# Performance work log

Measured on AMD Instinct MI355X. Metric: run time of the kernel, lower is better.

The kernel has to match this reference:

```python
import jax, jax.numpy as jnp
import numpy as np

D_MODEL = 1024
N_HEADS = 16
D_K = D_MODEL // N_HEADS
ROPE_BASE = 10000.0


def _rope_cos_sin(seq_len, dim):
    # matches calc_rope_theta: freqs over even indices of head dim
    freqs = jnp.arange(0, dim, 2, dtype=jnp.float32) / dim
    inv_freq = 1.0 / (ROPE_BASE ** freqs)                      # [dim/2]
    pos = jnp.arange(seq_len, dtype=jnp.float32)               # [S]
    ang = pos[:, None] * inv_freq[None, :]                     # [S, dim/2]
    return jnp.cos(ang), jnp.sin(ang)


def _apply_rope(x, cos, sin):
    # x: [N, S, dk]; complex pairs are consecutive elements (view_as_complex)
    x0 = x[..., 0::2]
    x1 = x[..., 1::2]
    r = x0 * cos - x1 * sin
    i = x0 * sin + x1 * cos
    return jnp.stack([r, i], axis=-1).reshape(x.shape)


def setup_inputs() -> dict:
    key = jax.random.key(0)
    ks = jax.random.split(key, 11)
    B, S, D = 4, 1024, D_MODEL
    w = lambda k: jax.random.normal(k, (D, D), dtype=jnp.float32) * 0.02
    b = lambda k: jax.random.normal(k, (D,), dtype=jnp.float32) * 0.02
    return {
        "q": jax.random.normal(ks[0], (B, S, D), dtype=jnp.float32),
        "k": jax.random.normal(ks[1], (B, S, D), dtype=jnp.float32),
        "v": jax.random.normal(ks[2], (B, S, D), dtype=jnp.float32),
        "Wq": w(ks[3]), "bq": b(ks[4]),
        "Wk": w(ks[5]), "bk": b(ks[6]),
        "Wv": w(ks[7]), "bv": b(ks[8]),
        "Wo": w(ks[9]), "bo": b(ks[10]),
    }


def reference(q, k, v, Wq, bq, Wk, bk, Wv, bv, Wo, bo):
    B, S, D = q.shape
    H, dk = N_HEADS, D_K
    qp = (q @ Wq + bq).reshape(B, S, H, dk)
    kp = (k @ Wk + bk).reshape(B, S, H, dk)
    vp = (v @ Wv + bv).reshape(B, S, H, dk)

    cos, sin = _rope_cos_sin(S, dk)
    # Faithful to source: raw reshape (B,S,H,dk)->(-1,S,dk) before RoPE
    qp = _apply_rope(qp.reshape(-1, S, dk), cos, sin).reshape(B, S, H, dk)
    kp = _apply_rope(kp.reshape(-1, S, dk), cos, sin).reshape(B, S, H, dk)

    qh = qp.transpose(0, 2, 1, 3)  # [B,H,S,dk]
    kh = kp.transpose(0, 2, 1, 3)
    vh = vp.transpose(0, 2, 1, 3)

    scores = jnp.einsum("bhqd,bhkd->bhqk", qh, kh) / jnp.sqrt(jnp.float32(dk))
    attn = jax.nn.softmax(scores, axis=-1)
    out = jnp.einsum("bhqk,bhkd->bhqd", attn, vh)
    out = out.transpose(0, 2, 1, 3).reshape(B, S, D)
    return out @ Wo + bo
```

## Files before the change

### kernel.cpp

```cpp
#include <hip/hip_runtime.h>

typedef __attribute__((ext_vector_type(8))) short bf16x8;
typedef __attribute__((ext_vector_type(4))) short short4v;
typedef __attribute__((ext_vector_type(4))) float f32x4;
typedef __attribute__((ext_vector_type(2))) unsigned u32x2;

#define MFMA16x16x32(a, b, c) __builtin_amdgcn_mfma_f32_16x16x32_bf16((a), (b), (c), 0, 0, 0)

__device__ __forceinline__ short f2bf(float f) {
    unsigned u = __builtin_bit_cast(unsigned, f);
    u += 0x7FFFu + ((u >> 16) & 1u);
    return (short)(u >> 16);
}

__device__ __forceinline__ unsigned cvtpk(float lo, float hi) {
    unsigned r;
    asm("v_cvt_pk_bf16_f32 %0, %1, %2" : "=v"(r) : "v"(lo), "v"(hi));
    return r;
}

__device__ __forceinline__ void gl_lds16(const void* g, void* l) {
    __builtin_amdgcn_global_load_lds((__attribute__((address_space(1))) void*)g,
                                     (__attribute__((address_space(3))) void*)l,
                                     16, 0, 0);
}

__device__ __forceinline__ void cvt16(const float* __restrict__ p, bf16x8& lo, bf16x8& hi) {
    f32x4 a = *(const f32x4*)(p);
    f32x4 b = *(const f32x4*)(p + 4);
    f32x4 c = *(const f32x4*)(p + 8);
    f32x4 d = *(const f32x4*)(p + 12);
#pragma unroll
    for (int i = 0; i < 4; ++i) {
        lo[i]     = f2bf(a[i]);
        lo[i + 4] = f2bf(b[i]);
        hi[i]     = f2bf(c[i]);
        hi[i + 4] = f2bf(d[i]);
    }
}

__global__ __launch_bounds__(256) void cvt3(const float* __restrict__ x0,
                                            const float* __restrict__ x1,
                                            const float* __restrict__ x2,
                                            short* __restrict__ y) {
    int sel = blockIdx.y;
    const float* x = sel == 0 ? x0 : (sel == 1 ? x1 : x2);
    short* yy = y + (size_t)sel * (1 << 22);
    int i = (blockIdx.x * 256 + threadIdx.x) * 16;
    bf16x8 lo, hi;
    cvt16(x + i, lo, hi);
    *(bf16x8*)(yy + i)     = lo;
    *(bf16x8*)(yy + i + 8) = hi;
}

__global__ __launch_bounds__(256) void transW4(const float* __restrict__ w0,
                                               const float* __restrict__ w1,
                                               const float* __restrict__ w2,
                                               const float* __restrict__ w3,
                                               short* __restrict__ wt) {
    __shared__ short t[64][80];
    int z = blockIdx.z;
    const float* W = z == 0 ? w0 : (z == 1 ? w1 : (z == 2 ? w2 : w3));
    short* Wt = wt + (size_t)z * (1 << 20);
    int bx = blockIdx.x, by = blockIdx.y;
    int tid = threadIdx.x;
    int sr = tid >> 2, sc = (tid & 3) * 16;
    bf16x8 lo, hi;
    cvt16(W + (by * 64 + sr) * 1024 + bx * 64 + sc, lo, hi);
    *(bf16x8*)&t[sr][sc]     = lo;
    *(bf16x8*)&t[sr][sc + 8] = hi;
    __syncthreads();
    bf16x8 o0, o1;
#pragma unroll
    for (int i = 0; i < 8; ++i) {
        o0[i] = t[sc + i][sr];
        o1[i] = t[sc + 8 + i][sr];
    }
    short* dst = Wt + (bx * 64 + sr) * 1024 + by * 64 + sc;
    *(bf16x8*)(dst)     = o0;
    *(bf16x8*)(dst + 8) = o1;
}

template <int MODE, int NZ>
__global__ __launch_bounds__(512) void gemm128(const short* __restrict__ A0,
                                               const short* __restrict__ A1,
                                               const short* __restrict__ Bt0,
                                               const short* __restrict__ Bt1,
                                               const float* __restrict__ b0,
                                               const float* __restrict__ b1,
                                               void* __restrict__ d0,
                                               void* __restrict__ d1) {
    __shared__ short As[3][128 * 64];
    __shared__ short Bs[3][128 * 64];
    const int K = 1024;
    int flat = blockIdx.x;
    int xcd = flat & 7, j = flat >> 3;
    int bm = xcd * 4 + (j & 3);
    int bn = (j >> 2) & 7;
    int z  = (NZ == 2) ? (j >> 5) : 0;
    const short* A    = z ? A1 : A0;
    const short* Bt   = z ? Bt1 : Bt0;
    const float* bias = z ? b1 : b0;
    void* dstv        = z ? d1 : d0;

    int tid = threadIdx.x;
    int wave = tid >> 6, lane = tid & 63;
    int quad = lane >> 4, l16 = lane & 15;
    int wm = (wave >> 2) * 64, wn = (wave & 3) * 32;
    int swr = l16 & 7;

    f32x4 acc[4][2] = {};

    auto stage = [&](int b, int t) {
        int kb = t * 64;
#pragma unroll
        for (int jj = 0; jj < 2; ++jj) {
            int c = jj * 512 + tid;
            int row = c >> 3, sl = c & 7;
            gl_lds16(A + (bm * 128 + row) * K + kb + ((sl ^ (row & 7)) * 8),
                     &As[b][c * 8]);
        }
#pragma unroll
        for (int jj = 0; jj < 2; ++jj) {
            int c = jj * 512 + tid;
            int row = c >> 3, sl = c & 7;
            gl_lds16(Bt + (bn * 128 + row) * K + kb + ((sl ^ (row & 7)) * 8),
                     &Bs[b][c * 8]);
        }
    };

    stage(0, 0);
    stage(1, 1);

    int cur = 0;
    for (int t = 0; t < 16; ++t) {
        asm volatile("s_waitcnt vmcnt(4)" ::: "memory");
        __builtin_amdgcn_sched_barrier(0);
        __builtin_amdgcn_s_barrier();
        __builtin_amdgcn_sched_barrier(0);
        int pre = cur >= 1 ? cur - 1 : 2;
        stage(pre, (t + 2) & 15);
#pragma unroll
        for (int ks = 0; ks < 2; ++ks) {
            bf16x8 bf[2], af[4];
#pragma unroll
            for (int ni = 0; ni < 2; ++ni)
                bf[ni] = *(const bf16x8*)
                    &Bs[cur][(wn + ni * 16 + l16) * 64 + (((ks * 4 + quad) ^ swr) * 8)];
#pragma unroll
            for (int mi = 0; mi < 4; ++mi)
                af[mi] = *(const bf16x8*)
                    &As[cur][(wm + mi * 16 + l16) * 64 + (((ks * 4 + quad) ^ swr) * 8)];
            __builtin_amdgcn_s_setprio(1);
#pragma unroll
            for (int mi = 0; mi < 4; ++mi)
#pragma unroll
                for (int ni = 0; ni < 2; ++ni)
                    acc[mi][ni] = MFMA16x16x32(af[mi], bf[ni], acc[mi][ni]);
            __builtin_amdgcn_s_setprio(0);
        }
        cur = cur < 2 ? cur + 1 : 0;
    }

    int row0 = bm * 128 + wm;
    int col0 = bn * 128 + wn;
#pragma unroll
    for (int mi = 0; mi < 4; ++mi) {
#pragma unroll
        for (int ni = 0; ni < 2; ++ni) {
            int gn = col0 + ni * 16 + l16;
            float bv = bias[gn];
            f32x4 c = acc[mi][ni];
            if constexpr (MODE == 0) {
                short* dst = (short*)dstv;
                int h = gn >> 6, dd = gn & 63;
                float inv = exp2f(-(float)(dd >> 1) * 0.41524101186092029f);
#pragma unroll
                for (int r = 0; r < 4; ++r) {
                    int gm = row0 + mi * 16 + quad * 4 + r;
                    int s = gm & 1023, b = gm >> 10;
                    int p = ((s << 4) + h) & 1023;
                    float val = c[r] + bv;
                    float partner = __shfl_xor(val, 1);
                    float sn, cs;
                    __sincosf((float)p * inv, &sn, &cs);
                    float res = (dd & 1) ? fmaf(partner, sn, val * cs)
                                         : fmaf(val, cs, -(partner * sn));
                    dst[((b * 16 + h) * 1024 + s) * 64 + dd] = f2bf(res);
                }
            } else if constexpr (MODE == 2) {
                short* dst = (short*)dstv;
                int h = gn >> 6, dd = gn & 63;
                int gm0 = row0 + mi * 16 + quad * 4;
                int s0 = gm0 & 1023, b = gm0 >> 10;
                short4v pack;
#pragma unroll
                for (int r = 0; r < 4; ++r) pack[r] = f2bf(c[r] + bv);
                *(short4v*)&dst[((b * 16 + h) * 64 + dd) * 1024 + s0] = pack;
            } else {
                float* dst = (float*)dstv;
#pragma unroll
                for (int r = 0; r < 4; ++r) {
                    int gm = row0 + mi * 16 + quad * 4 + r;
                    dst[gm * 1024 + gn] = c[r] + bv;
                }
            }
        }
    }
}

__global__ __launch_bounds__(512) void attn_kernel(const short* __restrict__ Qh,
                                                   const short* __restrict__ Kh,
                                                   const short* __restrict__ Vt,
                                                   short* __restrict__ O) {
    __shared__ short Ks[2][32 * 64];
    __shared__ short Vs[2][64 * 32];
    __shared__ short Pl[8][16 * 40];
    int tid = threadIdx.x;
    int wave = tid >> 6, lane = tid & 63;
    int quad = lane >> 4, l16 = lane & 15;
    int bh = blockIdx.x & 63, qt = blockIdx.x >> 6;
    int qrow = qt * 128 + wave * 16;

    const short* Qp = Qh + (bh * 1024 + qrow) * 64;
    bf16x8 aq[2];
#pragma unroll
    for (int kh = 0; kh < 2; ++kh)
        aq[kh] = *(const bf16x8*)&Qp[l16 * 64 + kh * 32 + quad * 8];

    const short* Kp = Kh + bh * 1024 * 64;
    const short* Vp = Vt + bh * 64 * 1024;

    int ck = tid & 255;
    bool isV = tid >= 256;
    int krow = ck >> 3;
    int vrow = ck >> 2;
    int ksrc = krow * 64 + (((ck & 7) ^ (krow & 7)) * 8);
    int vsrc = vrow * 1024 + ((((ck & 3) ^ (vrow & 3) ^ ((vrow >> 2) & 3)) & 3) * 8);

    int ksw  = l16 & 7;
    int vswr = (l16 & 3) ^ ((l16 >> 2) & 3);

    float lsum = 0.f;
    f32x4 oa[4] = {};

    if (!isV) gl_lds16(Kp + ksrc, &Ks[0][ck * 8]);
    else      gl_lds16(Vp + vsrc, &Vs[0][ck * 8]);
    __syncthreads();

    short* Pw = &Pl[wave][0];

    for (int kb = 0; kb < 1024; kb += 32) {
        int cur = (kb >> 5) & 1, nxt = cur ^ 1;
        int kb2 = (kb + 32) & 1023;
        if (!isV) gl_lds16(Kp + kb2 * 64 + ksrc, &Ks[nxt][ck * 8]);
        else      gl_lds16(Vp + kb2 + vsrc,      &Vs[nxt][ck * 8]);

#pragma unroll
        for (int g = 0; g < 2; ++g) {
            f32x4 s = {};
            __builtin_amdgcn_s_setprio(1);
#pragma unroll
            for (int kh = 0; kh < 2; ++kh) {
                bf16x8 ak = *(const bf16x8*)
                    &Ks[cur][(g * 16 + l16) * 64 + (((kh * 4 + quad) ^ ksw) * 8)];
                s = MFMA16x16x32(ak, aq[kh], s);
            }
            __builtin_amdgcn_s_setprio(0);
            float p[4];
#pragma unroll
            for (int r = 0; r < 4; ++r) {
                p[r] = exp2f(s[r] * 0.18033688011112042f);
                lsum += p[r];
            }
            u32x2 w;
            w[0] = cvtpk(p[0], p[1]);
            w[1] = cvtpk(p[2], p[3]);
            *(u32x2*)&Pw[l16 * 40 + g * 16 + quad * 4] = w;
        }

        bf16x8 bv[4];
#pragma unroll
        for (int t = 0; t < 4; ++t)
            bv[t] = *(const bf16x8*)&Vs[cur][(t * 16 + l16) * 32 + ((quad ^ vswr) * 8)];

        asm volatile("s_waitcnt lgkmcnt(0)" ::: "memory");
        bf16x8 ap = *(const bf16x8*)&Pw[l16 * 40 + quad * 8];

        __builtin_amdgcn_s_setprio(1);
#pragma unroll
        for (int t = 0; t < 4; ++t)
            oa[t] = MFMA16x16x32(ap, bv[t], oa[t]);
        __builtin_amdgcn_s_setprio(0);

        __syncthreads();
    }

    lsum += __shfl_xor(lsum, 16);
    lsum += __shfl_xor(lsum, 32);
    float inv[4];
#pragma unroll
    for (int r = 0; r < 4; ++r)
        inv[r] = 1.0f / __shfl(lsum, (lane & 48) + ((lane >> 4) & 3) * 4 + r);

    int b = bh >> 4, h = bh & 15;
#pragma unroll
    for (int t = 0; t < 4; ++t)
#pragma unroll
        for (int r = 0; r < 4; ++r) {
            int s = qrow + quad * 4 + r;
            O[(b * 1024 + s) * 1024 + h * 64 + t * 16 + l16] = f2bf(oa[t][r] * inv[r]);
        }
}

extern "C" void kernel_launch(void* const* d_in, const int* in_sizes, int n_in,
                              void* d_out, int out_size, void* d_ws, size_t ws_size,
                              hipStream_t stream) {
    const float* q  = (const float*)d_in[0];
    const float* k  = (const float*)d_in[1];
    const float* v  = (const float*)d_in[2];
    const float* Wq = (const float*)d_in[3];
    const float* bq = (const float*)d_in[4];
    const float* Wk = (const float*)d_in[5];
    const float* bk = (const float*)d_in[6];
    const float* Wv = (const float*)d_in[7];
    const float* bv = (const float*)d_in[8];
    const float* Wo = (const float*)d_in[9];
    const float* bo = (const float*)d_in[10];

    short* qb   = (short*)d_ws;
    short* kbuf = qb + (4 << 20);
    short* vb   = kbuf + (4 << 20);
    short* wt   = vb + (4 << 20);
    short* wtq  = wt;
    short* wtk  = wt + (1 << 20);
    short* wtv  = wt + (2 << 20);
    short* wto  = wt + (3 << 20);
    short* vt   = qb;
    short* obuf = kbuf;

    short* qh  = (short*)d_out;
    short* kh  = qh + (4 << 20);
    float* out = (float*)d_out;

    cvt3<<<dim3(1024, 3), 256, 0, stream>>>(q, k, v, qb);
    transW4<<<dim3(16, 16, 4), 256, 0, stream>>>(Wq, Wk, Wv, Wo, wt);

    gemm128<0, 2><<<512, 512, 0, stream>>>(qb, kbuf, wtq, wtk, bq, bk, qh, kh);
    gemm128<2, 1><<<256, 512, 0, stream>>>(vb, vb, wtv, wtv, bv, bv, vt, vt);

    attn_kernel<<<512, 512, 0, stream>>>(qh, kh, vt, obuf);

    gemm128<3, 1><<<256, 512, 0, stream>>>(obuf, obuf, wto, wto, bo, bo, out, out);
}
```

Measured before the change: 212.2 us.

## Merge prep kernels, batch QKV GEMMs, triple-buffer attention K/V loads

Combines the input conversion and weight transpose into one prep launch. It also fuses the Q/K and V projection GEMMs into a single 768-block launch when the workspace is large enough, so fewer launches run and the grid fills more CUs. The attention loop moves from a double buffer with a trailing __syncthreads to a three-stage LDS ring with vmcnt waits and one barrier per iteration, prefetching two tiles ahead. The price is more LDS per attention block, possible occupancy loss, and a workspace-size-dependent code path.

```diff
diff --git a/kernel.cpp b/kernel.cpp
--- a/kernel.cpp
+++ b/kernel.cpp
@@ -39,31 +39,32 @@
     }
 }
 
-__global__ __launch_bounds__(256) void cvt3(const float* __restrict__ x0,
-                                            const float* __restrict__ x1,
-                                            const float* __restrict__ x2,
-                                            short* __restrict__ y) {
-    int sel = blockIdx.y;
-    const float* x = sel == 0 ? x0 : (sel == 1 ? x1 : x2);
-    short* yy = y + (size_t)sel * (1 << 22);
-    int i = (blockIdx.x * 256 + threadIdx.x) * 16;
-    bf16x8 lo, hi;
-    cvt16(x + i, lo, hi);
-    *(bf16x8*)(yy + i)     = lo;
-    *(bf16x8*)(yy + i + 8) = hi;
-}
-
-__global__ __launch_bounds__(256) void transW4(const float* __restrict__ w0,
-                                               const float* __restrict__ w1,
-                                               const float* __restrict__ w2,
-                                               const float* __restrict__ w3,
-                                               short* __restrict__ wt) {
+__global__ __launch_bounds__(256) void prep(const float* __restrict__ q,
+                                            const float* __restrict__ k,
+                                            const float* __restrict__ v,
+                                            const float* __restrict__ w0,
+                                            const float* __restrict__ w1,
+                                            const float* __restrict__ w2,
+                                            const float* __restrict__ w3,
+                                            short* __restrict__ y,
+                                            short* __restrict__ wt) {
     __shared__ short t[64][80];
-    int z = blockIdx.z;
+    int bid = blockIdx.x, tid = threadIdx.x;
+    if (bid < 3072) {
+        int sel = bid >> 10;
+        const float* x = sel == 0 ? q : (sel == 1 ? k : v);
+        short* yy = y + (size_t)sel * (1 << 22);
+        int i = ((bid & 1023) * 256 + tid) * 16;
+        bf16x8 lo, hi;
+        cvt16(x + i, lo, hi);
+        *(bf16x8*)(yy + i)     = lo;
+        *(bf16x8*)(yy + i + 8) = hi;
+        return;
+    }
+    int tz = bid - 3072;
+    int z = tz >> 8, rem = tz & 255, bx = rem & 15, by = rem >> 4;
     const float* W = z == 0 ? w0 : (z == 1 ? w1 : (z == 2 ? w2 : w3));
     short* Wt = wt + (size_t)z * (1 << 20);
-    int bx = blockIdx.x, by = blockIdx.y;
-    int tid = threadIdx.x;
     int sr = tid >> 2, sc = (tid & 3) * 16;
     bf16x8 lo, hi;
     cvt16(W + (by * 64 + sr) * 1024 + bx * 64 + sc, lo, hi);
@@ -81,15 +82,17 @@
     *(bf16x8*)(dst + 8) = o1;
 }
 
-template <int MODE, int NZ>
-__global__ __launch_bounds__(512) void gemm128(const short* __restrict__ A0,
-                                               const short* __restrict__ A1,
-                                               const short* __restrict__ Bt0,
-                                               const short* __restrict__ Bt1,
-                                               const float* __restrict__ b0,
-                                               const float* __restrict__ b1,
-                                               void* __restrict__ d0,
-                                               void* __restrict__ d1) {
+__global__ __launch_bounds__(512) void gemm_qkv(const short* __restrict__ A0,
+                                                const short* __restrict__ A1,
+                                                const short* __restrict__ A2,
+                                                const short* __restrict__ wt,
+                                                const float* __restrict__ b0,
+                                                const float* __restrict__ b1,
+                                                const float* __restrict__ b2,
+                                                short* __restrict__ d0,
+                                                short* __restrict__ d1,
+                                                short* __restrict__ d2,
+                                                int zoff) {
     __shared__ short As[3][128 * 64];
     __shared__ short Bs[3][128 * 64];
     const int K = 1024;
@@ -97,11 +100,11 @@
     int xcd = flat & 7, j = flat >> 3;
     int bm = xcd * 4 + (j & 3);
     int bn = (j >> 2) & 7;
-    int z  = (NZ == 2) ? (j >> 5) : 0;
-    const short* A    = z ? A1 : A0;
-    const short* Bt   = z ? Bt1 : Bt0;
-    const float* bias = z ? b1 : b0;
-    void* dstv        = z ? d1 : d0;
+    int z  = zoff + (j >> 5);
+    const short* A    = z == 0 ? A0 : (z == 1 ? A1 : A2);
+    const short* Bt   = wt + (size_t)z * (1 << 20);
+    const float* bias = z == 0 ? b0 : (z == 1 ? b1 : b2);
+    short* dst        = z == 0 ? d0 : (z == 1 ? d1 : d2);
 
     int tid = threadIdx.x;
     int wave = tid >> 6, lane = tid & 63;
@@ -171,9 +174,8 @@
             int gn = col0 + ni * 16 + l16;
             float bv = bias[gn];
             f32x4 c = acc[mi][ni];
-            if constexpr (MODE == 0) {
-                short* dst = (short*)dstv;
-                int h = gn >> 6, dd = gn & 63;
+            int h = gn >> 6, dd = gn & 63;
+            if (z < 2) {
                 float inv = exp2f(-(float)(dd >> 1) * 0.41524101186092029f);
 #pragma unroll
                 for (int r = 0; r < 4; ++r) {
@@ -188,22 +190,102 @@
                                          : fmaf(val, cs, -(partner * sn));
                     dst[((b * 16 + h) * 1024 + s) * 64 + dd] = f2bf(res);
                 }
-            } else if constexpr (MODE == 2) {
-                short* dst = (short*)dstv;
-                int h = gn >> 6, dd = gn & 63;
+            } else {
                 int gm0 = row0 + mi * 16 + quad * 4;
                 int s0 = gm0 & 1023, b = gm0 >> 10;
                 short4v pack;
 #pragma unroll
                 for (int r = 0; r < 4; ++r) pack[r] = f2bf(c[r] + bv);
                 *(short4v*)&dst[((b * 16 + h) * 64 + dd) * 1024 + s0] = pack;
-            } else {
-                float* dst = (float*)dstv;
-#pragma unroll
-                for (int r = 0; r < 4; ++r) {
-                    int gm = row0 + mi * 16 + quad * 4 + r;
-                    dst[gm * 1024 + gn] = c[r] + bv;
-                }
+            }
+        }
+    }
+}
+
+__global__ __launch_bounds__(512) void gemm_o(const short* __restrict__ A,
+                                              const short* __restrict__ Bt,
+                                              const float* __restrict__ bias,
+                                              float* __restrict__ dst) {
+    __shared__ short As[3][128 * 64];
+    __shared__ short Bs[3][128 * 64];
+    const int K = 1024;
+    int flat = blockIdx.x;
+    int xcd = flat & 7, j = flat >> 3;
+    int bm = xcd * 4 + (j & 3);
+    int bn = (j >> 2) & 7;
+
+    int tid = threadIdx.x;
+    int wave = tid >> 6, lane = tid & 63;
+    int quad = lane >> 4, l16 = lane & 15;
+    int wm = (wave >> 2) * 64, wn = (wave & 3) * 32;
+    int swr = l16 & 7;
+
+    f32x4 acc[4][2] = {};
+
+    auto stage = [&](int b, int t) {
+        int kb = t * 64;
+#pragma unroll
+        for (int jj = 0; jj < 2; ++jj) {
+            int c = jj * 512 + tid;
+            int row = c >> 3, sl = c & 7;
+            gl_lds16(A + (bm * 128 + row) * K + kb + ((sl ^ (row & 7)) * 8),
+                     &As[b][c * 8]);
+        }
+#pragma unroll
+        for (int jj = 0; jj < 2; ++jj) {
+            int c = jj * 512 + tid;
+            int row = c >> 3, sl = c & 7;
+            gl_lds16(Bt + (bn * 128 + row) * K + kb + ((sl ^ (row & 7)) * 8),
+                     &Bs[b][c * 8]);
+        }
+    };
+
+    stage(0, 0);
+    stage(1, 1);
+
+    int cur = 0;
+    for (int t = 0; t < 16; ++t) {
+        asm volatile("s_waitcnt vmcnt(4)" ::: "memory");
+        __builtin_amdgcn_sched_barrier(0);
+        __builtin_amdgcn_s_barrier();
+        __builtin_amdgcn_sched_barrier(0);
+        int pre = cur >= 1 ? cur - 1 : 2;
+        stage(pre, (t + 2) & 15);
+#pragma unroll
+        for (int ks = 0; ks < 2; ++ks) {
+            bf16x8 bf[2], af[4];
+#pragma unroll
+            for (int ni = 0; ni < 2; ++ni)
+                bf[ni] = *(const bf16x8*)
+                    &Bs[cur][(wn + ni * 16 + l16) * 64 + (((ks * 4 + quad) ^ swr) * 8)];
+#pragma unroll
+            for (int mi = 0; mi < 4; ++mi)
+                af[mi] = *(const bf16x8*)
+                    &As[cur][(wm + mi * 16 + l16) * 64 + (((ks * 4 + quad) ^ swr) * 8)];
+            __builtin_amdgcn_s_setprio(1);
+#pragma unroll
+            for (int mi = 0; mi < 4; ++mi)
+#pragma unroll
+                for (int ni = 0; ni < 2; ++ni)
+                    acc[mi][ni] = MFMA16x16x32(af[mi], bf[ni], acc[mi][ni]);
+            __builtin_amdgcn_s_setprio(0);
+        }
+        cur = cur < 2 ? cur + 1 : 0;
+    }
+
+    int row0 = bm * 128 + wm;
+    int col0 = bn * 128 + wn;
+#pragma unroll
+    for (int mi = 0; mi < 4; ++mi) {
+#pragma unroll
+        for (int ni = 0; ni < 2; ++ni) {
+            int gn = col0 + ni * 16 + l16;
+            float bv = bias[gn];
+            f32x4 c = acc[mi][ni];
+#pragma unroll
+            for (int r = 0; r < 4; ++r) {
+                int gm = row0 + mi * 16 + quad * 4 + r;
+                dst[gm * 1024 + gn] = c[r] + bv;
             }
         }
     }
@@ -213,8 +295,8 @@
                                                    const short* __restrict__ Kh,
                                                    const short* __restrict__ Vt,
                                                    short* __restrict__ O) {
-    __shared__ short Ks[2][32 * 64];
-    __shared__ short Vs[2][64 * 32];
+    __shared__ short Ks[3][32 * 64];
+    __shared__ short Vs[3][64 * 32];
     __shared__ short Pl[8][16 * 40];
     int tid = threadIdx.x;
     int wave = tid >> 6, lane = tid & 63;
@@ -244,17 +326,23 @@
     float lsum = 0.f;
     f32x4 oa[4] = {};
 
-    if (!isV) gl_lds16(Kp + ksrc, &Ks[0][ck * 8]);
-    else      gl_lds16(Vp + vsrc, &Vs[0][ck * 8]);
-    __syncthreads();
+    if (!isV) { gl_lds16(Kp + ksrc, &Ks[0][ck * 8]);
+                gl_lds16(Kp + 32 * 64 + ksrc, &Ks[1][ck * 8]); }
+    else      { gl_lds16(Vp + vsrc, &Vs[0][ck * 8]);
+                gl_lds16(Vp + 32 + vsrc, &Vs[1][ck * 8]); }
 
     short* Pw = &Pl[wave][0];
 
+    int cur = 0;
     for (int kb = 0; kb < 1024; kb += 32) {
-        int cur = (kb >> 5) & 1, nxt = cur ^ 1;
-        int kb2 = (kb + 32) & 1023;
-        if (!isV) gl_lds16(Kp + kb2 * 64 + ksrc, &Ks[nxt][ck * 8]);
-        else      gl_lds16(Vp + kb2 + vsrc,      &Vs[nxt][ck * 8]);
+        asm volatile("s_waitcnt vmcnt(1)" ::: "memory");
+        __builtin_amdgcn_sched_barrier(0);
+        __builtin_amdgcn_s_barrier();
+        __builtin_amdgcn_sched_barrier(0);
+        int pre = cur >= 1 ? cur - 1 : 2;
+        int kb2 = (kb + 64) & 1023;
+        if (!isV) gl_lds16(Kp + kb2 * 64 + ksrc, &Ks[pre][ck * 8]);
+        else      gl_lds16(Vp + kb2 + vsrc,      &Vs[pre][ck * 8]);
 
 #pragma unroll
         for (int g = 0; g < 2; ++g) {
@@ -293,7 +381,7 @@
             oa[t] = MFMA16x16x32(ap, bv[t], oa[t]);
         __builtin_amdgcn_s_setprio(0);
 
-        __syncthreads();
+        cur = cur < 2 ? cur + 1 : 0;
     }
 
     lsum += __shfl_xor(lsum, 16);
@@ -332,24 +420,29 @@
     short* kbuf = qb + (4 << 20);
     short* vb   = kbuf + (4 << 20);
     short* wt   = vb + (4 << 20);
-    short* wtq  = wt;
-    short* wtk  = wt + (1 << 20);
-    short* wtv  = wt + (2 << 20);
     short* wto  = wt + (3 << 20);
-    short* vt   = qb;
     short* obuf = kbuf;
 
     short* qh  = (short*)d_out;
     short* kh  = qh + (4 << 20);
     float* out = (float*)d_out;
 
-    cvt3<<<dim3(1024, 3), 256, 0, stream>>>(q, k, v, qb);
-    transW4<<<dim3(16, 16, 4), 256, 0, stream>>>(Wq, Wk, Wv, Wo, wt);
-
-    gemm128<0, 2><<<512, 512, 0, stream>>>(qb, kbuf, wtq, wtk, bq, bk, qh, kh);
-    gemm128<2, 1><<<256, 512, 0, stream>>>(vb, vb, wtv, wtv, bv, bv, vt, vt);
+    bool batch3 = ws_size >= ((size_t)40 << 20);
+    short* vt = batch3 ? qb + (16 << 20) : qb;
+
+    prep<<<4096, 256, 0, stream>>>(q, k, v, Wq, Wk, Wv, Wo, qb, wt);
+
+    if (batch3) {
+        gemm_qkv<<<768, 512, 0, stream>>>(qb, kbuf, vb, wt, bq, bk, bv,
+                                          qh, kh, vt, 0);
+    } else {
+        gemm_qkv<<<512, 512, 0, stream>>>(qb, kbuf, vb, wt, bq, bk, bv,
+                                          qh, kh, vt, 0);
+        gemm_qkv<<<256, 512, 0, stream>>>(qb, kbuf, vb, wt, bq, bk, bv,
+                                          qh, kh, vt, 2);
+    }
 
     attn_kernel<<<512, 512, 0, stream>>>(qh, kh, vt, obuf);
 
-    gemm128<3, 1><<<256, 512, 0, stream>>>(obuf, obuf, wto, wto, bo, bo, out, out);
-}
+    gemm_o<<<256, 512, 0, stream>>>(obuf, wto, bo, out);
+}
```

Result: no change. 211.2 us (-0.5%).
